# Kernel tuning notes

Measured on AMD Instinct MI355X. Metric: run time of the kernel, lower is better.

Reference implementation:

```python
import jax, jax.numpy as jnp
import numpy as np
import math

B, S, D = 4, 2048, 1024


def setup_inputs() -> dict:
    key = jax.random.key(0)
    k1, k2, k3 = jax.random.split(key, 3)
    X = jax.random.normal(k1, (B, S, D), dtype=jnp.float32)
    # causal mask, broadcast over batch (True = keep)
    mask = jnp.broadcast_to(jnp.tril(jnp.ones((S, S), dtype=bool)), (B, S, S))
    # torch nn.Linear weights: y = x @ W.T; init scale ~ 1/sqrt(D)
    WQK = jax.random.normal(k2, (D, D), dtype=jnp.float32) / math.sqrt(D)
    WOV = jax.random.normal(k3, (D, D), dtype=jnp.float32) / math.sqrt(D)
    return {"X": X, "mask": mask, "WQK": WQK, "WOV": WOV}


def reference(X, mask, WQK, WOV):
    d = X.shape[-1]
    Q = jnp.einsum('bsd,ed->bse', X, WQK)          # WQK(X) = X @ WQK.T
    Sc = jnp.einsum('bse,bte->bst', Q, X)          # shared-QK scores: Q @ X^T
    # NOTE: original multiplies by sqrt(d_model) (not divide) - faithful
    Sc = Sc * jnp.asarray(math.sqrt(d), Sc.dtype)
    Sc = jnp.where(mask, Sc, -jnp.inf)
    A = jax.nn.softmax(Sc, axis=-1)                # dropout p=0.0 -> identity
    V = jnp.einsum('bsd,ed->bse', X, WOV)          # WOV(X)
    Y = jnp.einsum('bst,bte->bse', A, V)
    return (X + Y, A)
```

## Files before the change

kernel.cpp:

```cpp
#include <hip/hip_runtime.h>
#include <hip/hip_fp16.h>
#include <math.h>

typedef _Float16 half_t;
typedef _Float16 h8_t __attribute__((ext_vector_type(8)));
typedef _Float16 h4_t __attribute__((ext_vector_type(4)));
typedef float f4_t __attribute__((ext_vector_type(4)));

#define MFMA16(a, b, c) __builtin_amdgcn_mfma_f32_16x16x32_f16(a, b, c, 0, 0, 0)

static constexpr int kB = 4;
static constexpr int kS = 2048;
static constexpr int kD = 1024;
static constexpr int BM = 128;
static constexpr int BN = 128;
static constexpr int BK = 32;

__device__ __forceinline__ void gload16(const half_t* g, half_t* l) {
  __builtin_amdgcn_global_load_lds(
      (const __attribute__((address_space(1))) void*)g,
      (__attribute__((address_space(3))) void*)l, 16, 0, 0);
}

__device__ __forceinline__ void stage_tile(half_t* __restrict__ sm,
                                           const half_t* __restrict__ g, int ld) {
  const int t = threadIdx.x;
  const int r = t >> 2;
  const int c = (t & 3) * 8;
  gload16(&g[(size_t)r * ld + c], &sm[r * BK + c]);
  gload16(&g[(size_t)(r + 64) * ld + c], &sm[(r + 64) * BK + c]);
}

template <bool SPLIT>
__device__ __forceinline__ void gemm_core(const half_t* __restrict__ Ahi,
                                          const half_t* __restrict__ Alo, int lda,
                                          const half_t* __restrict__ Bhi,
                                          const half_t* __restrict__ Blo, int ldb,
                                          int k_iters, half_t* sm, f4_t acc[4][4]) {
  half_t* sAh = sm;
  half_t* sBh = sm + BM * BK;
  half_t* sAl = sm + 2 * BM * BK;
  half_t* sBl = sm + 3 * BM * BK;
  const int lane = threadIdx.x & 63;
  const int wid = threadIdx.x >> 6;
  const int wm = (wid >> 1) * 64;
  const int wn = (wid & 1) * 64;
  const int fr = lane & 15;
  const int fk = (lane >> 4) * 8;

  for (int kk = 0; kk < k_iters; ++kk) {
    const size_t ko = (size_t)kk * BK;
    stage_tile(sAh, Ahi + ko, lda);
    stage_tile(sBh, Bhi + ko, ldb);
    if (SPLIT) {
      stage_tile(sAl, Alo + ko, lda);
      stage_tile(sBl, Blo + ko, ldb);
    }
    __syncthreads();
    h8_t a[4], b[4], al[4], bl[4];
#pragma unroll
    for (int i = 0; i < 4; ++i) {
      a[i] = *(h8_t*)&sAh[(wm + i * 16 + fr) * BK + fk];
      b[i] = *(h8_t*)&sBh[(wn + i * 16 + fr) * BK + fk];
      if (SPLIT) {
        al[i] = *(h8_t*)&sAl[(wm + i * 16 + fr) * BK + fk];
        bl[i] = *(h8_t*)&sBl[(wn + i * 16 + fr) * BK + fk];
      }
    }
#pragma unroll
    for (int i = 0; i < 4; ++i)
#pragma unroll
      for (int j = 0; j < 4; ++j) {
        acc[i][j] = MFMA16(a[i], b[j], acc[i][j]);
        if (SPLIT) {
          acc[i][j] = MFMA16(a[i], bl[j], acc[i][j]);
          acc[i][j] = MFMA16(al[i], b[j], acc[i][j]);
        }
      }
    __syncthreads();
  }
}

__global__ __launch_bounds__(256) void gemm_q_kernel(
    const half_t* __restrict__ Xhi, const half_t* __restrict__ Xlo,
    const half_t* __restrict__ Whi, const half_t* __restrict__ Wlo,
    half_t* __restrict__ Qhi, half_t* __restrict__ Qlo) {
  __shared__ half_t sm[4 * BM * BK];
  const size_t arow = (size_t)blockIdx.y * BM;
  const size_t brow = (size_t)blockIdx.x * BN;
  f4_t acc[4][4] = {};
  gemm_core<true>(Xhi + arow * kD, Xlo + arow * kD, kD,
                  Whi + brow * kD, Wlo + brow * kD, kD, kD / BK, sm, acc);
  const int lane = threadIdx.x & 63;
  const int wid = threadIdx.x >> 6;
  const int wm = (wid >> 1) * 64, wn = (wid & 1) * 64;
  const int c16 = lane & 15, r4 = (lane >> 4) * 4;
#pragma unroll
  for (int i = 0; i < 4; ++i)
#pragma unroll
    for (int j = 0; j < 4; ++j)
#pragma unroll
      for (int r = 0; r < 4; ++r) {
        const size_t row = arow + wm + i * 16 + r4 + r;
        const size_t col = brow + wn + j * 16 + c16;
        const float q = acc[i][j][r];
        const half_t qh = (half_t)q;
        const half_t ql = (half_t)(q - (float)qh);
        const size_t idx = row * kD + col;
        Qhi[idx] = qh;
        Qlo[idx] = ql;
      }
}

__global__ __launch_bounds__(256) void gemm_v_kernel(
    const half_t* __restrict__ Xhi, const half_t* __restrict__ Whi,
    half_t* __restrict__ Vt) {
  __shared__ half_t sm[2 * BM * BK];
  const size_t arow = (size_t)blockIdx.y * BM;
  const size_t brow = (size_t)blockIdx.x * BN;
  f4_t acc[4][4] = {};
  gemm_core<false>(Xhi + arow * kD, nullptr, kD, Whi + brow * kD, nullptr, kD,
                   kD / BK, sm, acc);
  const int lane = threadIdx.x & 63;
  const int wid = threadIdx.x >> 6;
  const int wm = (wid >> 1) * 64, wn = (wid & 1) * 64;
  const int c16 = lane & 15, r4 = (lane >> 4) * 4;
#pragma unroll
  for (int i = 0; i < 4; ++i)
#pragma unroll
    for (int j = 0; j < 4; ++j)
#pragma unroll
      for (int r = 0; r < 4; ++r) {
        const size_t row = arow + wm + i * 16 + r4 + r;
        const size_t col = brow + wn + j * 16 + c16;
        const size_t bi = row >> 11;
        const size_t s = row & 2047;
        Vt[bi * (size_t)kD * kS + col * kS + s] = (half_t)acc[i][j][r];
      }
}

__global__ __launch_bounds__(256) void gemm_score_kernel(
    const half_t* __restrict__ Qhi, const half_t* __restrict__ Qlo,
    const half_t* __restrict__ Xhi, const half_t* __restrict__ Xlo,
    float* __restrict__ Sc) {
  const int tn = blockIdx.x, tm = blockIdx.y, bi = blockIdx.z;
  if (tn > tm) return;
  __shared__ half_t sm[4 * BM * BK];
  const size_t arow = (size_t)bi * kS + (size_t)tm * BM;
  const size_t brow = (size_t)bi * kS + (size_t)tn * BN;
  f4_t acc[4][4] = {};
  gemm_core<true>(Qhi + arow * kD, Qlo + arow * kD, kD,
                  Xhi + brow * kD, Xlo + brow * kD, kD, kD / BK, sm, acc);
  float* out = Sc + (size_t)bi * kS * kS;
  const int lane = threadIdx.x & 63;
  const int wid = threadIdx.x >> 6;
  const int wm = (wid >> 1) * 64, wn = (wid & 1) * 64;
  const int c16 = lane & 15, r4 = (lane >> 4) * 4;
#pragma unroll
  for (int i = 0; i < 4; ++i)
#pragma unroll
    for (int j = 0; j < 4; ++j)
#pragma unroll
      for (int r = 0; r < 4; ++r) {
        const int row = tm * BM + wm + i * 16 + r4 + r;
        const int col = tn * BN + wn + j * 16 + c16;
        out[(size_t)row * kS + col] = 32.0f * acc[i][j][r];
      }
}

__global__ __launch_bounds__(256) void softmax_kernel(float* __restrict__ A,
                                                      half_t* __restrict__ Ah) {
  const int rgl = blockIdx.x;
  const int s = rgl & 2047;
  float* row = A + (size_t)rgl * kS;
  half_t* hrow = Ah + (size_t)rgl * kS;
  const int tid = threadIdx.x;
  const int n = s + 1;
  float v[8];
  float mx = -INFINITY;
#pragma unroll
  for (int i = 0; i < 8; ++i) {
    const int t = tid + i * 256;
    v[i] = (t < n) ? row[t] : -INFINITY;
    mx = fmaxf(mx, v[i]);
  }
  for (int off = 32; off; off >>= 1) mx = fmaxf(mx, __shfl_xor(mx, off));
  __shared__ float red[8];
  const int lane = tid & 63, wid = tid >> 6;
  if (lane == 0) red[wid] = mx;
  __syncthreads();
  if (tid == 0) {
    float m = fmaxf(fmaxf(red[0], red[1]), fmaxf(red[2], red[3]));
    red[4] = m;
  }
  __syncthreads();
  mx = red[4];
  float sum = 0.0f;
#pragma unroll
  for (int i = 0; i < 8; ++i) {
    v[i] = (tid + i * 256 < n) ? __expf(v[i] - mx) : 0.0f;
    sum += v[i];
  }
  for (int off = 32; off; off >>= 1) sum += __shfl_xor(sum, off);
  __syncthreads();
  if (lane == 0) red[wid] = sum;
  __syncthreads();
  if (tid == 0) red[5] = 1.0f / (red[0] + red[1] + red[2] + red[3]);
  __syncthreads();
  const float inv = red[5];
#pragma unroll
  for (int i = 0; i < 8; ++i) {
    const int t = tid + i * 256;
    const float a = v[i] * inv;
    row[t] = a;
    hrow[t] = (half_t)a;
  }
}

__global__ __launch_bounds__(256) void gemm_y_kernel(
    const half_t* __restrict__ Ah, const half_t* __restrict__ Vt,
    const float* __restrict__ X, float* __restrict__ Out) {
  __shared__ half_t sm[2 * BM * BK];
  const int tn = blockIdx.x, tm = blockIdx.y, bi = blockIdx.z;
  const size_t abase = ((size_t)bi * kS + (size_t)tm * BM) * kS;
  const size_t bbase = ((size_t)bi * kD + (size_t)tn * BN) * kS;
  f4_t acc[4][4] = {};
  gemm_core<false>(Ah + abase, nullptr, kS, Vt + bbase, nullptr, kS,
                   (tm + 1) * BM / BK, sm, acc);
  const size_t obase = (size_t)bi * kS * kD;
  const int lane = threadIdx.x & 63;
  const int wid = threadIdx.x >> 6;
  const int wm = (wid >> 1) * 64, wn = (wid & 1) * 64;
  const int c16 = lane & 15, r4 = (lane >> 4) * 4;
#pragma unroll
  for (int i = 0; i < 4; ++i)
#pragma unroll
    for (int j = 0; j < 4; ++j)
#pragma unroll
      for (int r = 0; r < 4; ++r) {
        const size_t row = (size_t)tm * BM + wm + i * 16 + r4 + r;
        const size_t col = (size_t)tn * BN + wn + j * 16 + c16;
        const size_t idx = obase + row * kD + col;
        Out[idx] = X[idx] + acc[i][j][r];
      }
}

__global__ __launch_bounds__(256) void split_kernel(const float* __restrict__ x,
                                                    half_t* __restrict__ hi,
                                                    half_t* __restrict__ lo, int n4) {
  const int i = blockIdx.x * 256 + threadIdx.x;
  if (i >= n4) return;
  const float4 v = ((const float4*)x)[i];
  const float vv[4] = {v.x, v.y, v.z, v.w};
  h4_t h, l;
#pragma unroll
  for (int j = 0; j < 4; ++j) {
    const half_t hh = (half_t)vv[j];
    h[j] = hh;
    l[j] = (half_t)(vv[j] - (float)hh);
  }
  ((h4_t*)hi)[i] = h;
  ((h4_t*)lo)[i] = l;
}

__global__ __launch_bounds__(256) void cvt_kernel(const float* __restrict__ x,
                                                  half_t* __restrict__ hi, int n4) {
  const int i = blockIdx.x * 256 + threadIdx.x;
  if (i >= n4) return;
  const float4 v = ((const float4*)x)[i];
  h4_t h;
  h[0] = (half_t)v.x; h[1] = (half_t)v.y; h[2] = (half_t)v.z; h[3] = (half_t)v.w;
  ((h4_t*)hi)[i] = h;
}

extern "C" void kernel_launch(void* const* d_in, const int* in_sizes, int n_in,
                              void* d_out, int out_size, void* d_ws, size_t ws_size,
                              hipStream_t stream) {
  const float* X   = (const float*)d_in[0];
  const float* WQK = (const float*)d_in[2];
  const float* WOV = (const float*)d_in[3];

  constexpr size_t nX = (size_t)kB * kS * kD;
  constexpr size_t nW = (size_t)kD * kD;
  constexpr size_t nA = (size_t)kB * kS * kS;

  float* out0 = (float*)d_out;
  float* outA = out0 + nX;

  half_t* ws = (half_t*)d_ws;
  half_t* Xhi = ws; ws += nX;
  half_t* Xlo = ws; ws += nX;
  half_t* Qhi = ws; ws += nX;
  half_t* Qlo = ws; ws += nX;
  half_t* Whi = ws; ws += nW;
  half_t* Wlo = ws; ws += nW;
  half_t* WVh = ws; ws += nW;
  half_t* Vt  = ws; ws += nX;
  half_t* Ah  = ws; ws += nA;
  const size_t need_bytes = (size_t)((char*)ws - (char*)d_ws);
  if (ws_size < need_bytes) return;

  split_kernel<<<(int)(nX / 4 / 256), 256, 0, stream>>>(X, Xhi, Xlo, (int)(nX / 4));
  split_kernel<<<(int)(nW / 4 / 256), 256, 0, stream>>>(WQK, Whi, Wlo, (int)(nW / 4));
  cvt_kernel<<<(int)(nW / 4 / 256), 256, 0, stream>>>(WOV, WVh, (int)(nW / 4));

  gemm_q_kernel<<<dim3(kD / BN, kB * kS / BM), 256, 0, stream>>>(Xhi, Xlo, Whi, Wlo, Qhi, Qlo);
  gemm_v_kernel<<<dim3(kD / BN, kB * kS / BM), 256, 0, stream>>>(Xhi, WVh, Vt);
  gemm_score_kernel<<<dim3(kS / BN, kS / BM, kB), 256, 0, stream>>>(Qhi, Qlo, Xhi, Xlo, outA);
  softmax_kernel<<<kB * kS, 256, 0, stream>>>(outA, Ah);
  gemm_y_kernel<<<dim3(kD / BN, kS / BM, kB), 256, 0, stream>>>(Ah, Vt, X, out0);
}
```

Measured before the change: 418.1 us.

## Double-buffer LDS tiles in GEMM core and schedule heavy Y tiles first

The shared GEMM loop now uses two LDS buffers and issues the async global-to-LDS loads for the next K step before running MFMAs on the current one. This overlaps memory latency with compute and drops one barrier per iteration. It doubles LDS use per block, which may lower occupancy. The Y GEMM also reverses its row-tile order so the longest causal tiles launch first, improving load balance.

```diff
diff --git a/kernel.cpp b/kernel.cpp
--- a/kernel.cpp
+++ b/kernel.cpp
@@ -32,15 +32,25 @@
 }
 
 template <bool SPLIT>
+__device__ __forceinline__ void stage_all(half_t* buf, const half_t* Ahi,
+                                          const half_t* Alo, int lda,
+                                          const half_t* Bhi, const half_t* Blo,
+                                          int ldb, size_t ko) {
+  stage_tile(buf, Ahi + ko, lda);
+  stage_tile(buf + BM * BK, Bhi + ko, ldb);
+  if (SPLIT) {
+    stage_tile(buf + 2 * BM * BK, Alo + ko, lda);
+    stage_tile(buf + 3 * BM * BK, Blo + ko, ldb);
+  }
+}
+
+template <bool SPLIT>
 __device__ __forceinline__ void gemm_core(const half_t* __restrict__ Ahi,
                                           const half_t* __restrict__ Alo, int lda,
                                           const half_t* __restrict__ Bhi,
                                           const half_t* __restrict__ Blo, int ldb,
                                           int k_iters, half_t* sm, f4_t acc[4][4]) {
-  half_t* sAh = sm;
-  half_t* sBh = sm + BM * BK;
-  half_t* sAl = sm + 2 * BM * BK;
-  half_t* sBl = sm + 3 * BM * BK;
+  constexpr int BUFSZ = (SPLIT ? 4 : 2) * BM * BK;
   const int lane = threadIdx.x & 63;
   const int wid = threadIdx.x >> 6;
   const int wm = (wid >> 1) * 64;
@@ -48,23 +58,28 @@
   const int fr = lane & 15;
   const int fk = (lane >> 4) * 8;
 
+  half_t* cur = sm;
+  half_t* nxt = sm + BUFSZ;
+
+  stage_all<SPLIT>(cur, Ahi, Alo, lda, Bhi, Blo, ldb, 0);
+  asm volatile("s_waitcnt vmcnt(0)" ::: "memory");
+  __builtin_amdgcn_s_barrier();
+
   for (int kk = 0; kk < k_iters; ++kk) {
-    const size_t ko = (size_t)kk * BK;
-    stage_tile(sAh, Ahi + ko, lda);
-    stage_tile(sBh, Bhi + ko, ldb);
-    if (SPLIT) {
-      stage_tile(sAl, Alo + ko, lda);
-      stage_tile(sBl, Blo + ko, ldb);
-    }
-    __syncthreads();
+    if (kk + 1 < k_iters)
+      stage_all<SPLIT>(nxt, Ahi, Alo, lda, Bhi, Blo, ldb, (size_t)(kk + 1) * BK);
+    const half_t* sAh = cur;
+    const half_t* sBh = cur + BM * BK;
+    const half_t* sAl = cur + 2 * BM * BK;
+    const half_t* sBl = cur + 3 * BM * BK;
     h8_t a[4], b[4], al[4], bl[4];
 #pragma unroll
     for (int i = 0; i < 4; ++i) {
-      a[i] = *(h8_t*)&sAh[(wm + i * 16 + fr) * BK + fk];
-      b[i] = *(h8_t*)&sBh[(wn + i * 16 + fr) * BK + fk];
+      a[i] = *(const h8_t*)&sAh[(wm + i * 16 + fr) * BK + fk];
+      b[i] = *(const h8_t*)&sBh[(wn + i * 16 + fr) * BK + fk];
       if (SPLIT) {
-        al[i] = *(h8_t*)&sAl[(wm + i * 16 + fr) * BK + fk];
-        bl[i] = *(h8_t*)&sBl[(wn + i * 16 + fr) * BK + fk];
+        al[i] = *(const h8_t*)&sAl[(wm + i * 16 + fr) * BK + fk];
+        bl[i] = *(const h8_t*)&sBl[(wn + i * 16 + fr) * BK + fk];
       }
     }
 #pragma unroll
@@ -77,7 +92,9 @@
           acc[i][j] = MFMA16(al[i], b[j], acc[i][j]);
         }
       }
-    __syncthreads();
+    asm volatile("s_waitcnt vmcnt(0)" ::: "memory");
+    __builtin_amdgcn_s_barrier();
+    half_t* t = cur; cur = nxt; nxt = t;
   }
 }
 
@@ -85,7 +102,7 @@
     const half_t* __restrict__ Xhi, const half_t* __restrict__ Xlo,
     const half_t* __restrict__ Whi, const half_t* __restrict__ Wlo,
     half_t* __restrict__ Qhi, half_t* __restrict__ Qlo) {
-  __shared__ half_t sm[4 * BM * BK];
+  __shared__ half_t sm[2 * 4 * BM * BK];
   const size_t arow = (size_t)blockIdx.y * BM;
   const size_t brow = (size_t)blockIdx.x * BN;
   f4_t acc[4][4] = {};
@@ -115,7 +132,7 @@
 __global__ __launch_bounds__(256) void gemm_v_kernel(
     const half_t* __restrict__ Xhi, const half_t* __restrict__ Whi,
     half_t* __restrict__ Vt) {
-  __shared__ half_t sm[2 * BM * BK];
+  __shared__ half_t sm[2 * 2 * BM * BK];
   const size_t arow = (size_t)blockIdx.y * BM;
   const size_t brow = (size_t)blockIdx.x * BN;
   f4_t acc[4][4] = {};
@@ -145,7 +162,7 @@
     float* __restrict__ Sc) {
   const int tn = blockIdx.x, tm = blockIdx.y, bi = blockIdx.z;
   if (tn > tm) return;
-  __shared__ half_t sm[4 * BM * BK];
+  __shared__ half_t sm[2 * 4 * BM * BK];
   const size_t arow = (size_t)bi * kS + (size_t)tm * BM;
   const size_t brow = (size_t)bi * kS + (size_t)tn * BN;
   f4_t acc[4][4] = {};
@@ -220,8 +237,9 @@
 __global__ __launch_bounds__(256) void gemm_y_kernel(
     const half_t* __restrict__ Ah, const half_t* __restrict__ Vt,
     const float* __restrict__ X, float* __restrict__ Out) {
-  __shared__ half_t sm[2 * BM * BK];
-  const int tn = blockIdx.x, tm = blockIdx.y, bi = blockIdx.z;
+  __shared__ half_t sm[2 * 2 * BM * BK];
+  const int tn = blockIdx.x, bi = blockIdx.z;
+  const int tm = (kS / BM - 1) - blockIdx.y;
   const size_t abase = ((size_t)bi * kS + (size_t)tm * BM) * kS;
   const size_t bbase = ((size_t)bi * kD + (size_t)tn * BN) * kS;
   f4_t acc[4][4] = {};
```

Result: faster. 391.5 us (-6.4%).
